# Kernel tuning notes

Hardware: AMD Instinct MI355X
Metric: run time of the kernel (lower is better)

The kernel has to match this reference:

```python
import jax, jax.numpy as jnp
import numpy as np

# promonet-derived constants
S = 64        # FARGAN_SUBFRAME_SIZE
NSUB = 4      # FARGAN_SUBFRAMES
HOP = 256     # HOPSIZE = S * NSUB
L = 512       # HOPSIZE * FARGAN_PREVIOUS_FRAMES
F = 193       # acoustic features (192) + pitch period channel
G = 64        # GLOBAL_CHANNELS
CH = F - 1 + G  # conditioning width = 256
B = 64
FRAMES = 100


def setup_inputs() -> dict:
    key = jax.random.key(0)
    ks = jax.random.split(key, 24)

    def w(k, o, i):
        return jax.random.normal(k, (o, i), jnp.float32) / np.sqrt(i).astype(np.float32)

    feat = jax.random.normal(ks[0], (B, F - 1, FRAMES), jnp.float32)
    # last channel is the pitch period (rounded to int inside the model)
    period = jax.random.randint(ks[1], (B, 1, FRAMES), 64, 300).astype(jnp.float32)
    features = jnp.concatenate([feat, period], axis=1)  # (B, F, FRAMES)
    return {
        "features": features,
        "global_features": jax.random.normal(ks[2], (B, G), jnp.float32),
        "previous_samples": 0.1 * jax.random.normal(ks[3], (B, L), jnp.float32),
        # conditioning network (3 bias-free linears, tanh after each)
        "Wc1": w(ks[4], CH, CH),
        "Wc2": w(ks[5], CH, CH),
        "Wc3": w(ks[6], 2 * HOP, CH),
        # framewise conv: linear over [subframe_input(4S+4), prev feat state(2S)]
        "Wfw": w(ks[7], S, 6 * S + 4),
        "Wfw_g": w(ks[8], S, S),
        # three GRU cells (bias-free), torch gate order r,z,n
        "Wih1": w(ks[9], 3 * S, 2 * S), "Whh1": w(ks[10], 3 * S, S),
        "Wih2": w(ks[11], 3 * S, 2 * S), "Whh2": w(ks[12], 3 * S, S),
        "Wih3": w(ks[13], 3 * S, 2 * S), "Whh3": w(ks[14], 3 * S, S),
        # GLU gates
        "Wg1": w(ks[15], S, S), "Wg2": w(ks[16], S, S), "Wg3": w(ks[17], S, S),
        "Wsg": w(ks[18], 2 * S, 2 * S),
        # skip dense + output
        "Wsd": w(ks[19], 2 * S, 5 * S),
        "Wout": w(ks[20], S, 2 * S),
    }


def _glu(x, Wg):
    return x * jax.nn.sigmoid(x @ Wg.T)


def _gru(x, h, Wih, Whh):
    gi = x @ Wih.T
    gh = h @ Whh.T
    ir, iz, inew = jnp.split(gi, 3, axis=-1)
    hr, hz, hnew = jnp.split(gh, 3, axis=-1)
    r = jax.nn.sigmoid(ir + hr)
    z = jax.nn.sigmoid(iz + hz)
    n = jnp.tanh(inew + r * hnew)
    return (1.0 - z) * n + z * h


def reference(features, global_features, previous_samples,
              Wc1, Wc2, Wc3, Wfw, Wfw_g,
              Wih1, Whh1, Wih2, Whh2, Wih3, Whh3,
              Wg1, Wg2, Wg3, Wsg, Wsd, Wout):
    Bn = features.shape[0]
    lb_ar = jnp.arange(S + 4)

    def subframe(feat2s, prev, period, states):
        s1, s2, s3, sfw = states
        prev_sub = prev[:, -S:]
        # data-dependent pitch lookback gather with wrap for short periods
        idx = L - period[:, None] + lb_ar[None, :] - 2
        idx = idx - period[:, None] * (idx >= L)
        lookback = jnp.take_along_axis(prev, idx, axis=1)  # (B, S+4)
        sub_in = jnp.concatenate([feat2s, prev_sub, lookback], axis=1)  # (B, 4S+4)
        fw = _glu(jnp.tanh(jnp.concatenate([sub_in, sfw], axis=1) @ Wfw.T), Wfw_g)
        g1 = _gru(jnp.concatenate([fw, prev_sub], 1), s1, Wih1, Whh1)
        o1 = _glu(g1, Wg1)
        g2 = _gru(jnp.concatenate([o1, prev_sub], 1), s2, Wih2, Whh2)
        o2 = _glu(g2, Wg2)
        g3 = _gru(jnp.concatenate([o2, prev_sub], 1), s3, Wih3, Whh3)
        o3 = _glu(g3, Wg3)
        skip = jnp.concatenate([o1, o2, o3, fw, prev_sub], 1)  # (B, 5S)
        so = _glu(jnp.tanh(skip @ Wsd.T), Wsg)
        out = jnp.tanh(so @ Wout.T)  # (B, S)
        return out, (g1, g2, g3, feat2s)

    def frame_step(carry, feat_t):
        prev, states = carry
        period = jnp.round(feat_t[:, -1]).astype(jnp.int32)
        x = jnp.concatenate([feat_t[:, :-1], global_features], axis=1)
        c = jnp.tanh(jnp.tanh(jnp.tanh(x @ Wc1.T) @ Wc2.T) @ Wc3.T)  # (B, 2*HOP)
        subs = c.reshape(Bn, 2 * S, NSUB)
        outs = []
        for k in range(NSUB):  # fixed tiny unroll over subframes
            out, states = subframe(subs[:, :, k], prev, period, states)
            prev = jnp.concatenate([prev[:, S:], out], axis=1)
            outs.append(out)
        return (prev, states), jnp.concatenate(outs, axis=1)  # (B, HOP)

    dt = features.dtype
    states0 = (jnp.zeros((Bn, S), dt), jnp.zeros((Bn, S), dt),
               jnp.zeros((Bn, S), dt), jnp.zeros((Bn, 2 * S), dt))
    feats_t = jnp.transpose(features, (2, 0, 1))  # (frames, B, F)
    _, sigs = jax.lax.scan(frame_step, (previous_samples, states0), feats_t)
    # (frames, B, HOP) -> (B, 1, frames*HOP)
    return jnp.transpose(sigs, (1, 0, 2)).reshape(Bn, 1, -1)
```

## Files before the change

### kernel.cpp

```cpp
#include <hip/hip_runtime.h>
#include <hip/hip_bf16.h>

#define SS      64
#define NSUB    4
#define LPREV   512
#define NF      193
#define NFRAMES 100
#define BATCH   64
#define RPW     16

typedef __attribute__((ext_vector_type(8))) short   short8;
typedef __attribute__((ext_vector_type(4))) float   floatx4;

__device__ __forceinline__ float bf2f(unsigned short u) {
    return __uint_as_float(((unsigned int)u) << 16);
}
__device__ __forceinline__ unsigned short f2bf(float x) {
    unsigned int u = __float_as_uint(x);
    return (unsigned short)((u + 0x7fffu + ((u >> 16) & 1u)) >> 16);
}
__device__ __forceinline__ unsigned int packbf(float a, float b) {
    return (unsigned int)f2bf(a) | ((unsigned int)f2bf(b) << 16);
}
__device__ __forceinline__ float fexp2(float x) {
#if __has_builtin(__builtin_amdgcn_exp2f)
    return __builtin_amdgcn_exp2f(x);
#else
    return exp2f(x);
#endif
}
__device__ __forceinline__ float frcp(float x) {
#if __has_builtin(__builtin_amdgcn_rcpf)
    return __builtin_amdgcn_rcpf(x);
#else
    return 1.0f / x;
#endif
}
__device__ __forceinline__ float fsig(float x) {
    return frcp(1.0f + fexp2(-1.442695041f * x));
}
__device__ __forceinline__ float ftanh(float x) {
    return fmaf(2.0f, frcp(1.0f + fexp2(-2.885390082f * x)), -1.0f);
}
__device__ __forceinline__ float ld1f(int f32, const void* p, size_t i) {
    if (f32) return ((const float*)p)[i];
    return bf2f(((const unsigned short*)p)[i]);
}
__device__ __forceinline__ float lo16(unsigned int u) { return __uint_as_float(u << 16); }
__device__ __forceinline__ float hi16(unsigned int u) { return __uint_as_float(u & 0xffff0000u); }

__device__ __forceinline__ floatx4 mf(short8 a, short8 b, floatx4 c) {
    return __builtin_amdgcn_mfma_f32_16x16x32_bf16(a, b, c, 0, 0, 0);
}

__device__ __forceinline__ short8 ldA(const unsigned short* buf, int strideU,
                                      int m, int kb, int q) {
    const unsigned int* p = (const unsigned int*)buf + m * strideU + kb * 16 + q * 4;
    uint4 u = *(const uint4*)p;
    return __builtin_bit_cast(short8, u);
}
__device__ __forceinline__ short8 ldB(const uint4* __restrict__ w, int idx) {
    return __builtin_bit_cast(short8, w[idx]);
}

#define OFF_FW   0
#define OFF_FWG  3328
#define OFF_GRU(G) (3840 + 4608*(G))
#define OFF_WG(G)  (17664 + 512*(G))
#define OFF_SD   19200
#define OFF_SG   24320
#define OFF_OUT  26368
#define NFRAG    27392

__global__ void fargan_detect(const void* feats, int* flag) {
    const float* pf = (const float*)feats;
    int ok = 1;
    for (int f = 0; f < 50; ++f) {
        float v = pf[192 * NFRAMES + f];
        if (!(v >= 63.0f && v <= 301.0f)) { ok = 0; break; }
    }
    *flag = ok;
}

__global__ __launch_bounds__(256) void fargan_prep(
    const int* __restrict__ flag,
    const void* Wfw, const void* Wfwg,
    const void* Wih1, const void* Whh1, const void* Wih2, const void* Whh2,
    const void* Wih3, const void* Whh3,
    const void* Wg1, const void* Wg2, const void* Wg3,
    const void* Wsg, const void* Wsd, const void* Wout,
    uint4* __restrict__ wbuf)
{
    int fi = blockIdx.x * 256 + threadIdx.x;
    if (fi >= NFRAG) return;
    int f32 = *flag;
    const void* mats[14] = {Wfw, Wfwg, Wih1, Whh1, Wih2, Whh2, Wih3, Whh3,
                            Wg1, Wg2, Wg3, Wsg, Wsd, Wout};
    const int NSEG = 20;
    const int sb[NSEG]  = {0,3328, 3840,5376,6912,7936, 8448,9984,11520,12544,
                           13056,14592,16128,17152, 17664,18176,18688, 19200,24320,26368};
    const int sa[NSEG]  = {0,1, 2,2,2,3, 4,4,4,5, 6,6,6,7, 8,9,10, 12,11,13};
    const int sbx[NSEG] = {-1,-1, 3,3,-1,-1, 5,5,-1,-1, 7,7,-1,-1, -1,-1,-1, -1,-1,-1};
    const int sro[NSEG] = {0,0, 0,64,128,128, 0,64,128,128, 0,64,128,128, 0,0,0, 0,0,0};
    const int skb[NSEG] = {13,2, 6,6,4,2, 6,6,4,2, 6,6,4,2, 2,2,2, 10,4,4};
    const int ska[NSEG] = {388,64, 128,128,128,64, 128,128,128,64, 128,128,128,64,
                           64,64,64, 320,128,128};
    const int skr[NSEG] = {388,64, 192,192,128,64, 192,192,128,64, 192,192,128,64,
                           64,64,64, 320,128,128};
    int s = 0;
    for (int i = 1; i < NSEG; ++i) if (fi >= sb[i]) s = i;
    int local = fi - sb[s];
    int ln = local & 15, lq = (local >> 4) & 3, tkb = local >> 6;
    int KB = skb[s];
    int kb = tkb % KB, tile = tkb / KB;
    int row = sro[s] + tile * 16 + ln;
    int Ka = ska[s], Kr = skr[s];
    union { unsigned short h[8]; uint4 v; } u;
#pragma unroll
    for (int j = 0; j < 8; ++j) {
        int k = kb * 32 + lq * 8 + j;
        unsigned short val = 0;
        if (k < Kr) {
            const void* m; size_t off;
            if (sbx[s] >= 0 && k >= Ka) { m = mats[sbx[s]]; off = (size_t)row * 64 + (k - Ka); }
            else                        { m = mats[sa[s]];  off = (size_t)row * Ka + k; }
            val = f32 ? f2bf(((const float*)m)[off]) : ((const unsigned short*)m)[off];
        }
        u.h[j] = val;
    }
    wbuf[fi] = u.v;
}

__global__ __launch_bounds__(256) void fargan_prep_conv(
    const int* __restrict__ flag,
    const void* Wc1, const void* Wc2, const void* Wc3,
    unsigned int* __restrict__ wct)
{
    int idx = blockIdx.x * 256 + threadIdx.x;
    if (idx >= 131072) return;
    int f32 = *flag;
    const void* W; int n, k2;
    if (idx < 32768)      { W = Wc1; k2 = idx >> 8, n = idx & 255; }
    else if (idx < 65536) { W = Wc2; k2 = (idx - 32768) >> 8; n = idx & 255; }
    else                  { W = Wc3; k2 = (idx - 65536) >> 9; n = (idx - 65536) & 511; }
    size_t off = (size_t)n * 256 + 2 * k2;
    unsigned int v;
    if (f32) {
        const float* p = (const float*)W + off;
        v = packbf(p[0], p[1]);
    } else {
        v = *(const unsigned int*)((const unsigned short*)W + off);
    }
    wct[idx] = v;
}

template<bool F32>
__device__ __forceinline__ void conv_body(
    const void* __restrict__ feats, const void* __restrict__ gfeat,
    const unsigned int* __restrict__ wct, unsigned short* __restrict__ cb16)
{
    int blk = blockIdx.x;
    int b = blk / NFRAMES, f = blk - b * NFRAMES;
    int t = threadIdx.x;
    __shared__ float xa[256], xb[256];

    float v;
    if (t < 192) v = ld1f(F32 ? 1 : 0, feats, (size_t)b * (NF * NFRAMES) + t * NFRAMES + f);
    else         v = ld1f(F32 ? 1 : 0, gfeat, (size_t)b * 64 + (t - 192));
    xa[t] = v;
    __syncthreads();

    const unsigned int* w1 = wct;
    const unsigned int* w2 = wct + 32768;
    const unsigned int* w3 = wct + 65536;

    float a0 = 0.f, a1 = 0.f;
#pragma unroll 8
    for (int k2 = 0; k2 < 128; ++k2) {
        unsigned int u = w1[k2 * 256 + t];
        a0 = fmaf(lo16(u), xa[2 * k2], a0);
        a1 = fmaf(hi16(u), xa[2 * k2 + 1], a1);
    }
    xb[t] = ftanh(a0 + a1);
    __syncthreads();

    a0 = 0.f; a1 = 0.f;
#pragma unroll 8
    for (int k2 = 0; k2 < 128; ++k2) {
        unsigned int u = w2[k2 * 256 + t];
        a0 = fmaf(lo16(u), xb[2 * k2], a0);
        a1 = fmaf(hi16(u), xb[2 * k2 + 1], a1);
    }
    xa[t] = ftanh(a0 + a1);
    __syncthreads();

    a0 = 0.f; a1 = 0.f;
    float b0 = 0.f, b1 = 0.f;
#pragma unroll 8
    for (int k2 = 0; k2 < 128; ++k2) {
        unsigned int u = w3[k2 * 512 + t];
        unsigned int u2 = w3[k2 * 512 + t + 256];
        a0 = fmaf(lo16(u),  xa[2 * k2],     a0);
        a1 = fmaf(hi16(u),  xa[2 * k2 + 1], a1);
        b0 = fmaf(lo16(u2), xa[2 * k2],     b0);
        b1 = fmaf(hi16(u2), xa[2 * k2 + 1], b1);
    }
    unsigned short* co = cb16 + ((size_t)b * NFRAMES + f) * 512;
    int e0 = t, e1 = t + 256;
    co[(e0 & 3) * 128 + (e0 >> 2)] = f2bf(ftanh(a0 + a1));
    co[(e1 & 3) * 128 + (e1 >> 2)] = f2bf(ftanh(b0 + b1));
}

__global__ __launch_bounds__(256) void fargan_conv(
    const void* feats, const void* gfeat,
    const int* flag, const unsigned int* wct, unsigned short* cb16)
{
    if (*flag) conv_body<true>(feats, gfeat, wct, cb16);
    else       conv_body<false>(feats, gfeat, wct, cb16);
}


__global__ __launch_bounds__(256, 1) void fargan_seq(
    const void* __restrict__ feats, const void* __restrict__ prev_in,
    const int* __restrict__ flag, const unsigned short* __restrict__ cb16,
    const uint4* __restrict__ wbuf, void* __restrict__ outp)
{
    const int t = threadIdx.x;
    const int b0 = blockIdx.x * RPW;
    const int lane = t & 63, w = t >> 6;
    const int lq = lane >> 4, ln = lane & 15;
    const int nj = 16 * w + ln;
    const int f32 = *flag;

    __shared__ __align__(16) unsigned short hist[RPW * 520];
    __shared__ __align__(16) unsigned short catb[RPW * 424];
    __shared__ __align__(16) unsigned short xg  [RPW * 200];
    __shared__ __align__(16) unsigned short skx [RPW * 328];
    __shared__ __align__(16) unsigned short sdbb[RPW * 136];
    __shared__ __align__(16) unsigned short sobb[RPW * 136];
    __shared__ __align__(16) unsigned short v64 [RPW * 72];
    __shared__ __align__(16) unsigned short wsd[128 * 328];
    __shared__ __align__(16) unsigned int   cframe[RPW * 260];
    __shared__ int period_s[RPW];

    short8 Bfw[13], Bfwg[2], Bout[4];
    short8 Br[3][6], Bz[3][6], Bi[3][4], Bh[3][2], Bg[3][2];
    short8 Bsg[2][4];
#pragma unroll
    for (int kb = 0; kb < 13; ++kb) Bfw[kb] = ldB(wbuf, OFF_FW + (w * 13 + kb) * 64 + lane);
#pragma unroll
    for (int kb = 0; kb < 2; ++kb)  Bfwg[kb] = ldB(wbuf, OFF_FWG + (w * 2 + kb) * 64 + lane);
#pragma unroll
    for (int G = 0; G < 3; ++G) {
        const int OR = OFF_GRU(G), OZ = OR + 1536, OI = OR + 3072, OH = OR + 4096;
#pragma unroll
        for (int kb = 0; kb < 6; ++kb) {
            Br[G][kb] = ldB(wbuf, OR + (w * 6 + kb) * 64 + lane);
            Bz[G][kb] = ldB(wbuf, OZ + (w * 6 + kb) * 64 + lane);
        }
#pragma unroll
        for (int kb = 0; kb < 4; ++kb) Bi[G][kb] = ldB(wbuf, OI + (w * 4 + kb) * 64 + lane);
#pragma unroll
        for (int kb = 0; kb < 2; ++kb) {
            Bh[G][kb] = ldB(wbuf, OH + (w * 2 + kb) * 64 + lane);
            Bg[G][kb] = ldB(wbuf, OFF_WG(G) + (w * 2 + kb) * 64 + lane);
        }
    }
#pragma unroll
    for (int tile = 0; tile < 2; ++tile)
#pragma unroll
        for (int kb = 0; kb < 4; ++kb)
            Bsg[tile][kb] = ldB(wbuf, OFF_SG + ((2 * w + tile) * 4 + kb) * 64 + lane);
#pragma unroll
    for (int kb = 0; kb < 4; ++kb) Bout[kb] = ldB(wbuf, OFF_OUT + (w * 4 + kb) * 64 + lane);

    for (int fi = t; fi < 8 * 10 * 64; fi += 256) {
        int lane2 = fi & 63, tkb = fi >> 6;
        int kb = tkb % 10, tile = tkb / 10;
        int lq2 = lane2 >> 4, ln2 = lane2 & 15;
        int row = tile * 16 + ln2;
        uint4 v = wbuf[OFF_SD + fi];
        *(uint4*)((unsigned int*)wsd + row * 164 + kb * 16 + lq2 * 4) = v;
    }

    for (int i = t; i < RPW * 424; i += 256) catb[i] = 0;
    for (int i = t; i < RPW * 200; i += 256) xg[i] = 0;
    for (int i = t; i < RPW * 328; i += 256) skx[i] = 0;
    for (int i = t; i < RPW * 136; i += 256) { sdbb[i] = 0; sobb[i] = 0; }
    for (int i = t; i < RPW * 72;  i += 256) v64[i] = 0;
    for (int i = t; i < RPW * 260; i += 256) cframe[i] = 0;
    for (int i = t; i < RPW * 512; i += 256) {
        int row = i >> 9, c = i & 511;
        hist[row * 520 + c] = f2bf(ld1f(f32, prev_in, (size_t)(b0 + row) * LPREV + c));
    }
    __syncthreads();
    for (int i = t; i < RPW * 64; i += 256) {
        int row = i >> 6, c = i & 63;
        unsigned short hh = hist[row * 520 + 448 + c];
        catb[row * 424 + 128 + c] = hh;
        skx [row * 328 + 256 + c] = hh;
        xg  [row * 200 + 64  + c] = hh;
    }

    floatx4 svr[3];
#pragma unroll
    for (int G = 0; G < 3; ++G) svr[G] = (floatx4){0.f, 0.f, 0.f, 0.f};
    __syncthreads();

    const floatx4 z4 = {0.f, 0.f, 0.f, 0.f};
    int base = 0;
    for (int f = 0; f < NFRAMES; ++f) {
        for (int i = t; i < RPW * 64; i += 256) {
            int row = i >> 6, j = i & 63;
            ((unsigned int*)catb)[row * 212 + 130 + j] = cframe[row * 260 + 192 + j];
        }
        __syncthreads();
        {
            int row = t >> 4, part = t & 15;
            const uint4* src = (const uint4*)(cb16 + ((size_t)(b0 + row) * NFRAMES + f) * 512)
                             + part * 4;
            uint4* dst = (uint4*)(cframe + row * 260) + part * 4;
            uint4 s0 = src[0], s1 = src[1], s2 = src[2], s3 = src[3];
            dst[0] = s0; dst[1] = s1; dst[2] = s2; dst[3] = s3;
        }
        if (t < RPW)
            period_s[t] = (int)rintf(ld1f(f32, feats,
                (size_t)(b0 + t) * (NF * NFRAMES) + (NF - 1) * NFRAMES + f));
        __syncthreads();

        for (int kk = 0; kk < NSUB; ++kk) {
            {
                int row = t >> 4, x16 = t & 15;
                unsigned int* cat32 = (unsigned int*)catb;
                int cb = row * 212;
                const unsigned int* cf = cframe + row * 260;
                int j4 = x16 * 4;
#pragma unroll
                for (int i = 0; i < 4; ++i) cat32[cb + j4 + i] = cf[kk * 64 + j4 + i];
                if (kk > 0) {
#pragma unroll
                    for (int i = 0; i < 4; ++i)
                        cat32[cb + 130 + j4 + i] = cf[(kk - 1) * 64 + j4 + i];
                }
                int per = period_s[row];
#pragma unroll
                for (int ii = 0; ii < 5; ++ii) {
                    int i = x16 * 5 + ii;
                    if (i < 68) {
                        int idx = LPREV - per + i - 2;
                        if (idx >= LPREV) idx -= per;
                        catb[row * 424 + 192 + i] = hist[row * 520 + ((base + idx) & 511)];
                    }
                }
            }
            __syncthreads();

            {
                floatx4 C0 = z4, C1 = z4;
#pragma unroll
                for (int kb = 0; kb < 13; ++kb) {
                    short8 a = ldA(catb, 212, ln, kb, lq);
                    if (kb & 1) C1 = mf(a, Bfw[kb], C1);
                    else        C0 = mf(a, Bfw[kb], C0);
                }
#pragma unroll
                for (int r = 0; r < 4; ++r) {
                    int m = 4 * lq + r;
                    v64[m * 72 + nj] = f2bf(ftanh(C0[r] + C1[r]));
                }
            }
            __syncthreads();

            {
                floatx4 C = z4;
#pragma unroll
                for (int kb = 0; kb < 2; ++kb)
                    C = mf(ldA(v64, 36, ln, kb, lq), Bfwg[kb], C);
#pragma unroll
                for (int r = 0; r < 4; ++r) {
                    int m = 4 * lq + r;
                    float vp = bf2f(v64[m * 72 + nj]);
                    unsigned short ob = f2bf(vp * fsig(C[r]));
                    skx[m * 328 + 192 + nj] = ob;
                    xg [m * 200 + nj]       = ob;
                    xg [m * 200 + 128 + nj] = f2bf(svr[0][r]);
                }
            }
            __syncthreads();

#pragma unroll
            for (int G = 0; G < 3; ++G) {
                {
                    floatx4 Cr = z4, Cz = z4, Ci = z4, Ch = z4;
#pragma unroll
                    for (int kb = 0; kb < 6; ++kb) {
                        short8 a = ldA(xg, 100, ln, kb, lq);
                        Cr = mf(a, Br[G][kb], Cr);
                        Cz = mf(a, Bz[G][kb], Cz);
                        if (kb < 4) Ci = mf(a, Bi[G][kb], Ci);
                        else        Ch = mf(a, Bh[G][kb - 4], Ch);
                    }
#pragma unroll
                    for (int r = 0; r < 4; ++r) {
                        int m = 4 * lq + r;
                        float rr = fsig(Cr[r]);
                        float zz = fsig(Cz[r]);
                        float nn = ftanh(Ci[r] + rr * Ch[r]);
                        float sn = fmaf(zz, svr[G][r] - nn, nn);
                        svr[G][r] = sn;
                        v64[m * 72 + nj] = f2bf(sn);
                    }
                }
                __syncthreads();
                {
                    floatx4 C = z4;
#pragma unroll
                    for (int kb = 0; kb < 2; ++kb)
                        C = mf(ldA(v64, 36, ln, kb, lq), Bg[G][kb], C);
#pragma unroll
                    for (int r = 0; r < 4; ++r) {
                        int m = 4 * lq + r;
                        unsigned short ob = f2bf(svr[G][r] * fsig(C[r]));
                        skx[m * 328 + G * 64 + nj] = ob;
                        if (G < 2) {
                            xg[m * 200 + nj]       = ob;
                            xg[m * 200 + 128 + nj] = f2bf(svr[G + 1][r]);
                        }
                    }
                }
                __syncthreads();
            }

            {
                floatx4 C00 = z4, C01 = z4, C10 = z4, C11 = z4;
                int n0 = 32 * w + ln, n1 = n0 + 16;
#pragma unroll
                for (int kb = 0; kb < 10; ++kb) {
                    short8 a   = ldA(skx, 164, ln, kb, lq);
                    short8 b0f = ldA(wsd, 164, n0, kb, lq);
                    short8 b1f = ldA(wsd, 164, n1, kb, lq);
                    if (kb & 1) { C01 = mf(a, b0f, C01); C11 = mf(a, b1f, C11); }
                    else        { C00 = mf(a, b0f, C00); C10 = mf(a, b1f, C10); }
                }
#pragma unroll
                for (int r = 0; r < 4; ++r) {
                    int m = 4 * lq + r;
                    sdbb[m * 136 + n0] = f2bf(ftanh(C00[r] + C01[r]));
                    sdbb[m * 136 + n1] = f2bf(ftanh(C10[r] + C11[r]));
                }
            }
            __syncthreads();

            {
                floatx4 C0 = z4, C1 = z4;
                int n0 = 32 * w + ln, n1 = n0 + 16;
#pragma unroll
                for (int kb = 0; kb < 4; ++kb) {
                    short8 a = ldA(sdbb, 68, ln, kb, lq);
                    C0 = mf(a, Bsg[0][kb], C0);
                    C1 = mf(a, Bsg[1][kb], C1);
                }
#pragma unroll
                for (int r = 0; r < 4; ++r) {
                    int m = 4 * lq + r;
                    float s0 = bf2f(sdbb[m * 136 + n0]);
                    float s1 = bf2f(sdbb[m * 136 + n1]);
                    sobb[m * 136 + n0] = f2bf(s0 * fsig(C0[r]));
                    sobb[m * 136 + n1] = f2bf(s1 * fsig(C1[r]));
                }
            }
            __syncthreads();

            {
                floatx4 C = z4;
#pragma unroll
                for (int kb = 0; kb < 4; ++kb)
                    C = mf(ldA(sobb, 68, ln, kb, lq), Bout[kb], C);
#pragma unroll
                for (int r = 0; r < 4; ++r) {
                    int m = 4 * lq + r;
                    float ov = ftanh(C[r]);
                    unsigned short ob = f2bf(ov);
                    hist[m * 520 + ((base + nj) & 511)] = ob;
                    catb[m * 424 + 128 + nj] = ob;
                    skx [m * 328 + 256 + nj] = ob;
                    xg  [m * 200 + 64  + nj] = ob;
                    if (f32) {
                        size_t oi = (size_t)(b0 + m) * (NFRAMES * NSUB * SS)
                                  + f * (NSUB * SS) + kk * SS + nj;
                        ((float*)outp)[oi] = ov;
                    }
                }
            }
            __syncthreads();

            base += SS;
        }

        if (!f32) {
            int row = t >> 4, x16 = t & 15;
            int fb2 = ((f & 1) ? 256 : 0) >> 1;
            const unsigned int* hsrc = (const unsigned int*)hist + row * 260 + fb2 + x16 * 8;
            uint4 v0 = *(const uint4*)(hsrc);
            uint4 v1 = *(const uint4*)(hsrc + 4);
            unsigned short* op = (unsigned short*)outp
                + (size_t)(b0 + row) * (NFRAMES * 256) + f * 256 + x16 * 16;
            *(uint4*)(op)     = v0;
            *(uint4*)(op + 8) = v1;
        }
    }
}

extern "C" void kernel_launch(void* const* d_in, const int* in_sizes, int n_in,
                              void* d_out, int out_size, void* d_ws, size_t ws_size,
                              hipStream_t stream) {
    const void* feats = d_in[0];
    const void* gfeat = d_in[1];
    const void* prev  = d_in[2];
    const void* Wc1   = d_in[3];
    const void* Wc2   = d_in[4];
    const void* Wc3   = d_in[5];
    const void* Wfw   = d_in[6];
    const void* Wfwg  = d_in[7];
    const void* Wih1  = d_in[8];
    const void* Whh1  = d_in[9];
    const void* Wih2  = d_in[10];
    const void* Whh2  = d_in[11];
    const void* Wih3  = d_in[12];
    const void* Whh3  = d_in[13];
    const void* Wg1   = d_in[14];
    const void* Wg2   = d_in[15];
    const void* Wg3   = d_in[16];
    const void* Wsg   = d_in[17];
    const void* Wsd   = d_in[18];
    const void* Wout  = d_in[19];

    int*            flag = (int*)d_ws;
    unsigned short* cb16 = (unsigned short*)((char*)d_ws + 256);
    unsigned int*   wct  = (unsigned int*)((char*)d_ws + 256 + 6553600);
    uint4*          wbuf = (uint4*)((char*)d_ws + 256 + 6553600 + 524288);

    fargan_detect<<<1, 1, 0, stream>>>(feats, flag);
    fargan_prep<<<(NFRAG + 255) / 256, 256, 0, stream>>>(flag, Wfw, Wfwg,
        Wih1, Whh1, Wih2, Whh2, Wih3, Whh3, Wg1, Wg2, Wg3, Wsg, Wsd, Wout, wbuf);
    fargan_prep_conv<<<512, 256, 0, stream>>>(flag, Wc1, Wc2, Wc3, wct);
    fargan_conv<<<BATCH * NFRAMES, 256, 0, stream>>>(feats, gfeat, flag, wct, cb16);
    fargan_seq<<<BATCH / RPW, 256, 0, stream>>>(feats, prev, flag, cb16, wbuf, d_out);
}
```

Before: 2.680 ms.

## Prefetch conditioning into registers and overlap skip-dense MFMAs with GRU stages

Removes the shared-memory cframe staging buffer. Each thread now holds the next subframe's conditioning slice in a register, loaded one subframe ahead, and the pitch period is loaded one frame ahead. This cuts one barrier and the per-frame copy. The skip-dense matmul is split so its partial K blocks accumulate during the three GRU stages, leaving only two blocks after them. The framewise conv uses four accumulators to shorten dependency chains, and bf16 output is written per subframe instead of copied from hist each frame. In exchange, register pressure rises from the extra accumulators and prefetch registers.

```diff
diff --git a/kernel.cpp b/kernel.cpp
--- a/kernel.cpp
+++ b/kernel.cpp
@@ -240,7 +240,6 @@
     __shared__ __align__(16) unsigned short sobb[RPW * 136];
     __shared__ __align__(16) unsigned short v64 [RPW * 72];
     __shared__ __align__(16) unsigned short wsd[128 * 328];
-    __shared__ __align__(16) unsigned int   cframe[RPW * 260];
     __shared__ int period_s[RPW];
 
     short8 Bfw[13], Bfwg[2], Bout[4];
@@ -288,7 +287,6 @@
     for (int i = t; i < RPW * 328; i += 256) skx[i] = 0;
     for (int i = t; i < RPW * 136; i += 256) { sdbb[i] = 0; sobb[i] = 0; }
     for (int i = t; i < RPW * 72;  i += 256) v64[i] = 0;
-    for (int i = t; i < RPW * 260; i += 256) cframe[i] = 0;
     for (int i = t; i < RPW * 512; i += 256) {
         int row = i >> 9, c = i & 511;
         hist[row * 520 + c] = f2bf(ld1f(f32, prev_in, (size_t)(b0 + row) * LPREV + c));
@@ -305,47 +303,54 @@
     floatx4 svr[3];
 #pragma unroll
     for (int G = 0; G < 3; ++G) svr[G] = (floatx4){0.f, 0.f, 0.f, 0.f};
+
+    const int prow = t >> 4, px16 = t & 15, pe8 = (t & 15) * 8;
+    uint4 pfc;
+    pfc = *(const uint4*)(cb16 + ((size_t)(b0 + prow) * NFRAMES + 0) * 512 + 0 * 128 + pe8);
+    float pper = 0.f;
+    if (t < RPW)
+        pper = ld1f(f32, feats, (size_t)(b0 + t) * (NF * NFRAMES) + (NF - 1) * NFRAMES + 0);
     __syncthreads();
 
     const floatx4 z4 = {0.f, 0.f, 0.f, 0.f};
     int base = 0;
     for (int f = 0; f < NFRAMES; ++f) {
-        for (int i = t; i < RPW * 64; i += 256) {
-            int row = i >> 6, j = i & 63;
-            ((unsigned int*)catb)[row * 212 + 130 + j] = cframe[row * 260 + 192 + j];
+        if (t < RPW) period_s[t] = (int)rintf(pper);
+        __syncthreads();
+        if (t < RPW) {
+            int fN = (f + 1 < NFRAMES) ? f + 1 : f;
+            pper = ld1f(f32, feats, (size_t)(b0 + t) * (NF * NFRAMES) + (NF - 1) * NFRAMES + fN);
         }
-        __syncthreads();
-        {
-            int row = t >> 4, part = t & 15;
-            const uint4* src = (const uint4*)(cb16 + ((size_t)(b0 + row) * NFRAMES + f) * 512)
-                             + part * 4;
-            uint4* dst = (uint4*)(cframe + row * 260) + part * 4;
-            uint4 s0 = src[0], s1 = src[1], s2 = src[2], s3 = src[3];
-            dst[0] = s0; dst[1] = s1; dst[2] = s2; dst[3] = s3;
-        }
-        if (t < RPW)
-            period_s[t] = (int)rintf(ld1f(f32, feats,
-                (size_t)(b0 + t) * (NF * NFRAMES) + (NF - 1) * NFRAMES + f));
-        __syncthreads();
 
         for (int kk = 0; kk < NSUB; ++kk) {
+            floatx4 SD00 = z4, SD01 = z4, SD10 = z4, SD11 = z4;
+            const int n0 = 32 * w + ln, n1 = n0 + 16;
+
             {
-                int row = t >> 4, x16 = t & 15;
+                int row = prow;
                 unsigned int* cat32 = (unsigned int*)catb;
                 int cb = row * 212;
-                const unsigned int* cf = cframe + row * 260;
-                int j4 = x16 * 4;
-#pragma unroll
-                for (int i = 0; i < 4; ++i) cat32[cb + j4 + i] = cf[kk * 64 + j4 + i];
-                if (kk > 0) {
-#pragma unroll
-                    for (int i = 0; i < 4; ++i)
-                        cat32[cb + 130 + j4 + i] = cf[(kk - 1) * 64 + j4 + i];
+                int u0 = pe8 >> 1;
+                unsigned int o0 = cat32[cb + u0 + 0];
+                unsigned int o1 = cat32[cb + u0 + 1];
+                unsigned int o2 = cat32[cb + u0 + 2];
+                unsigned int o3 = cat32[cb + u0 + 3];
+                cat32[cb + 130 + u0 + 0] = o0;
+                cat32[cb + 130 + u0 + 1] = o1;
+                cat32[cb + 130 + u0 + 2] = o2;
+                cat32[cb + 130 + u0 + 3] = o3;
+                *(uint4*)(cat32 + cb + u0) = pfc;
+                {
+                    int sN = f * 4 + kk + 1;
+                    if (sN > NFRAMES * 4 - 1) sN = NFRAMES * 4 - 1;
+                    int fN = sN >> 2, kN = sN & 3;
+                    pfc = *(const uint4*)(cb16
+                        + ((size_t)(b0 + row) * NFRAMES + fN) * 512 + kN * 128 + pe8);
                 }
                 int per = period_s[row];
 #pragma unroll
                 for (int ii = 0; ii < 5; ++ii) {
-                    int i = x16 * 5 + ii;
+                    int i = px16 * 5 + ii;
                     if (i < 68) {
                         int idx = LPREV - per + i - 2;
                         if (idx >= LPREV) idx -= per;
@@ -356,17 +361,21 @@
             __syncthreads();
 
             {
-                floatx4 C0 = z4, C1 = z4;
+                floatx4 C0 = z4, C1 = z4, C2 = z4, C3 = z4;
 #pragma unroll
                 for (int kb = 0; kb < 13; ++kb) {
                     short8 a = ldA(catb, 212, ln, kb, lq);
-                    if (kb & 1) C1 = mf(a, Bfw[kb], C1);
-                    else        C0 = mf(a, Bfw[kb], C0);
+                    switch (kb & 3) {
+                        case 0: C0 = mf(a, Bfw[kb], C0); break;
+                        case 1: C1 = mf(a, Bfw[kb], C1); break;
+                        case 2: C2 = mf(a, Bfw[kb], C2); break;
+                        default: C3 = mf(a, Bfw[kb], C3); break;
+                    }
                 }
 #pragma unroll
                 for (int r = 0; r < 4; ++r) {
                     int m = 4 * lq + r;
-                    v64[m * 72 + nj] = f2bf(ftanh(C0[r] + C1[r]));
+                    v64[m * 72 + nj] = f2bf(ftanh((C0[r] + C1[r]) + (C2[r] + C3[r])));
                 }
             }
             __syncthreads();
@@ -399,6 +408,21 @@
                         Cz = mf(a, Bz[G][kb], Cz);
                         if (kb < 4) Ci = mf(a, Bi[G][kb], Ci);
                         else        Ch = mf(a, Bh[G][kb - 4], Ch);
+                    }
+                    {
+                        int kbs = (G == 0) ? 6 : (G == 1) ? 0 : 2;
+                        int nkb = (G == 0) ? 4 : 2;
+#pragma unroll
+                        for (int j = 0; j < 4; ++j) {
+                            if (j < nkb) {
+                                int kb = kbs + j;
+                                short8 a   = ldA(skx, 164, ln, kb, lq);
+                                short8 b0f = ldA(wsd, 164, n0, kb, lq);
+                                short8 b1f = ldA(wsd, 164, n1, kb, lq);
+                                if (kb & 1) { SD01 = mf(a, b0f, SD01); SD11 = mf(a, b1f, SD11); }
+                                else        { SD00 = mf(a, b0f, SD00); SD10 = mf(a, b1f, SD10); }
+                            }
+                        }
                     }
 #pragma unroll
                     for (int r = 0; r < 4; ++r) {
@@ -432,28 +456,26 @@
             }
 
             {
-                floatx4 C00 = z4, C01 = z4, C10 = z4, C11 = z4;
-                int n0 = 32 * w + ln, n1 = n0 + 16;
-#pragma unroll
-                for (int kb = 0; kb < 10; ++kb) {
+#pragma unroll
+                for (int j = 0; j < 2; ++j) {
+                    int kb = 4 + j;
                     short8 a   = ldA(skx, 164, ln, kb, lq);
                     short8 b0f = ldA(wsd, 164, n0, kb, lq);
                     short8 b1f = ldA(wsd, 164, n1, kb, lq);
-                    if (kb & 1) { C01 = mf(a, b0f, C01); C11 = mf(a, b1f, C11); }
-                    else        { C00 = mf(a, b0f, C00); C10 = mf(a, b1f, C10); }
+                    if (kb & 1) { SD01 = mf(a, b0f, SD01); SD11 = mf(a, b1f, SD11); }
+                    else        { SD00 = mf(a, b0f, SD00); SD10 = mf(a, b1f, SD10); }
                 }
 #pragma unroll
                 for (int r = 0; r < 4; ++r) {
                     int m = 4 * lq + r;
-                    sdbb[m * 136 + n0] = f2bf(ftanh(C00[r] + C01[r]));
-                    sdbb[m * 136 + n1] = f2bf(ftanh(C10[r] + C11[r]));
+                    sdbb[m * 136 + n0] = f2bf(ftanh(SD00[r] + SD01[r]));
+                    sdbb[m * 136 + n1] = f2bf(ftanh(SD10[r] + SD11[r]));
                 }
             }
             __syncthreads();
 
             {
                 floatx4 C0 = z4, C1 = z4;
-                int n0 = 32 * w + ln, n1 = n0 + 16;
 #pragma unroll
                 for (int kb = 0; kb < 4; ++kb) {
                     short8 a = ldA(sdbb, 68, ln, kb, lq);
@@ -485,28 +507,15 @@
                     catb[m * 424 + 128 + nj] = ob;
                     skx [m * 328 + 256 + nj] = ob;
                     xg  [m * 200 + 64  + nj] = ob;
-                    if (f32) {
-                        size_t oi = (size_t)(b0 + m) * (NFRAMES * NSUB * SS)
-                                  + f * (NSUB * SS) + kk * SS + nj;
-                        ((float*)outp)[oi] = ov;
-                    }
+                    size_t oi = (size_t)(b0 + m) * (NFRAMES * NSUB * SS)
+                              + f * (NSUB * SS) + kk * SS + nj;
+                    if (f32) ((float*)outp)[oi] = ov;
+                    else     ((unsigned short*)outp)[oi] = ob;
                 }
             }
             __syncthreads();
 
             base += SS;
-        }
-
-        if (!f32) {
-            int row = t >> 4, x16 = t & 15;
-            int fb2 = ((f & 1) ? 256 : 0) >> 1;
-            const unsigned int* hsrc = (const unsigned int*)hist + row * 260 + fb2 + x16 * 8;
-            uint4 v0 = *(const uint4*)(hsrc);
-            uint4 v1 = *(const uint4*)(hsrc + 4);
-            unsigned short* op = (unsigned short*)outp
-                + (size_t)(b0 + row) * (NFRAMES * 256) + f * 256 + x16 * 16;
-            *(uint4*)(op)     = v0;
-            *(uint4*)(op + 8) = v1;
         }
     }
 }
```

Measured after the change: 2.613 ms. 1.03x faster.
